# Performance work log

Hardware: AMD Instinct MI355X
Metric: run time of the kernel (lower is better)

## Reference

```python
import jax, jax.numpy as jnp
import numpy as np

N = 100000   # nodes
E = 400000   # edges
R = 237      # relations
D = 200      # feature dim (dims=[200,200,200])
B = 4096     # triple batch
L = 2        # num GAT layers
ALPHA = 0.01 # leaky-relu slope


def setup_inputs() -> dict:
    key = jax.random.key(0)
    ks = jax.random.split(key, 11)
    return dict(
        ent_embed=jax.random.normal(ks[0], (N, D), jnp.float32),
        rel_embed=jax.random.normal(ks[1], (R, D), jnp.float32),
        W_gat=jax.random.normal(ks[2], (L, D, D), jnp.float32) * 0.1,
        att_a=jax.random.normal(ks[3], (L, 2 * D), jnp.float32) * 0.1,
        W_hw=jax.random.normal(ks[4], (D, D), jnp.float32) * 0.1,
        b_hw=jax.random.normal(ks[5], (1, D), jnp.float32) * 0.1,
        edge_src=jax.random.randint(ks[6], (E,), 0, N),
        edge_dst=jax.random.randint(ks[7], (E,), 0, N),
        batch_h=jax.random.randint(ks[8], (B,), 0, N),
        batch_r=jax.random.randint(ks[9], (B,), 0, R),
        batch_t=jax.random.randint(ks[10], (B,), 0, N),
    )


def _gat_layer(x, W, a, src, dst):
    # x: [N,D], W: [D,D], a: [2D]
    Wh = x @ W                                  # [N,D]
    s_src = Wh @ a[:D]                          # [N] source score
    s_dst = Wh @ a[D:]                          # [N] dest score
    e = jax.nn.leaky_relu(s_src[src] + s_dst[dst], ALPHA)  # [E]
    # segment softmax over incoming edges of each destination node
    m = jax.ops.segment_max(e, dst, num_segments=N)
    m = jax.lax.stop_gradient(jnp.where(jnp.isfinite(m), m, 0.0))
    ex = jnp.exp(e - m[dst])
    denom = jax.ops.segment_sum(ex, dst, num_segments=N)
    att = ex / jnp.maximum(denom[dst], 1e-9)    # [E]
    out = jax.ops.segment_sum(att[:, None] * Wh[src], dst, num_segments=N)  # [N,D]
    return jax.nn.sigmoid(out)                  # act = torch.sigmoid, 1 head, concat=False


def reference(ent_embed, rel_embed, W_gat, att_a, W_hw, b_hw,
              edge_src, edge_dst, batch_h, batch_r, batch_t):
    x = ent_embed
    for i in range(L):
        gat_out = _gat_layer(x, W_gat[i], att_a[i], edge_src, edge_dst)
        # highway gate: sigma = sigmoid(x W + b); shared W,b across layers
        sigma = jax.nn.sigmoid(x @ W_hw + b_hw)
        x = sigma * gat_out + (1.0 - sigma) * x
    h = x[batch_h]
    r = rel_embed[batch_r]
    t = x[batch_t]
    return (h, r, t)
```

## Files before the change

kernel.cpp:

```cpp
#include <hip/hip_runtime.h>
#include <math.h>

#define NNODES 100000
#define NEDGES 400000
#define DIM    200
#define NB     4096
#define NL     2
#define ALPHA  0.01f
#define D4     (DIM/4)
#define NPAD   100096
#define KPAD   224
#define NKS    7
#define NCF    26
#define NBB    (2*NB)

typedef __attribute__((ext_vector_type(8))) short short8;
typedef __attribute__((ext_vector_type(4))) float f32x4;

__device__ __forceinline__ float sigm(float v) { return 1.0f / (1.0f + expf(-v)); }
__device__ __forceinline__ unsigned short f2bf(float f) {
    unsigned u = __float_as_uint(f);
    unsigned r = u + 0x7fff + ((u >> 16) & 1);
    return (unsigned short)(r >> 16);
}
__device__ __forceinline__ float bflo(unsigned u) { return __uint_as_float(u << 16); }
__device__ __forceinline__ float bfhi(unsigned u) { return __uint_as_float(u & 0xffff0000u); }

__global__ __launch_bounds__(256) void zero2_k(int* __restrict__ a, int* __restrict__ b)
{
    int i = blockIdx.x * 256 + threadIdx.x;
    if (i < NNODES) { a[i] = 0; b[i] = 0; }
}

__global__ __launch_bounds__(256) void convscore_k(const float* __restrict__ xin,
                                                   const float* __restrict__ wvl,
                                                   unsigned short* __restrict__ ap,
                                                   float* __restrict__ s_src,
                                                   float* __restrict__ s_dst)
{
    int gt = blockIdx.x * 256 + threadIdx.x;
    int row = gt >> 5, hl = gt & 31;
    if (row >= NPAD) return;

    float ps = 0.f, pd = 0.f;
    if (hl < 28) {
        uint4 o = make_uint4(0u, 0u, 0u, 0u);
        if (row < NNODES && hl < 25) {
            size_t base = (size_t)row * D4 + hl * 2;
            float4 x0 = ((const float4*)xin)[base];
            float4 x1 = ((const float4*)xin)[base + 1];
            o.x = (unsigned)f2bf(x0.x) | ((unsigned)f2bf(x0.y) << 16);
            o.y = (unsigned)f2bf(x0.z) | ((unsigned)f2bf(x0.w) << 16);
            o.z = (unsigned)f2bf(x1.x) | ((unsigned)f2bf(x1.y) << 16);
            o.w = (unsigned)f2bf(x1.z) | ((unsigned)f2bf(x1.w) << 16);
            float4 s0 = ((const float4*)wvl)[hl * 2];
            float4 s1 = ((const float4*)wvl)[hl * 2 + 1];
            float4 d0 = ((const float4*)(wvl + DIM))[hl * 2];
            float4 d1 = ((const float4*)(wvl + DIM))[hl * 2 + 1];
            ps = x0.x*s0.x + x0.y*s0.y + x0.z*s0.z + x0.w*s0.w
               + x1.x*s1.x + x1.y*s1.y + x1.z*s1.z + x1.w*s1.w;
            pd = x0.x*d0.x + x0.y*d0.y + x0.z*d0.z + x0.w*d0.w
               + x1.x*d1.x + x1.y*d1.y + x1.z*d1.z + x1.w*d1.w;
        }
        ((uint4*)ap)[(size_t)row * 28 + hl] = o;
    }
#pragma unroll
    for (int m = 16; m; m >>= 1) {
        ps += __shfl_xor(ps, m, 32);
        pd += __shfl_xor(pd, m, 32);
    }
    if (hl == 0 && row < NNODES) { s_src[row] = ps; s_dst[row] = pd; }
}

__global__ void wpack_k(const float* __restrict__ Wg, const float* __restrict__ Whw,
                        unsigned short* __restrict__ wp)
{
    int t = blockIdx.x * 256 + threadIdx.x;
    if (t >= NKS * NCF * 64) return;
    int l = t & 63, cf = (t >> 6) % NCF, ks = t / (NCF * 64);
    int col = (cf % 13) * 16 + (l & 15);
    const float* W = (cf < 13) ? Wg : Whw;
    unsigned rr[4];
#pragma unroll
    for (int j = 0; j < 4; ++j) {
        int ka = ks * 32 + (l >> 4) * 8 + 2 * j;
        float fa = (ka < DIM && col < DIM) ? W[ka * DIM + col] : 0.f;
        float fb = (ka + 1 < DIM && col < DIM) ? W[(ka + 1) * DIM + col] : 0.f;
        rr[j] = (unsigned)f2bf(fa) | ((unsigned)f2bf(fb) << 16);
    }
    ((uint4*)wp)[t] = make_uint4(rr[0], rr[1], rr[2], rr[3]);
}

__global__ void wvec_k(const float* __restrict__ Wg, const float* __restrict__ aa,
                       float* __restrict__ wv)
{
    int t = blockIdx.x * 256 + threadIdx.x;
    if (t >= NL * 2 * DIM) return;
    int l = t / (2 * DIM), sd = (t / DIM) % 2, k = t % DIM;
    const float* W = Wg + (size_t)l * DIM * DIM + (size_t)k * DIM;
    const float* av = aa + (size_t)l * 2 * DIM + sd * DIM;
    float s = 0.f;
    for (int c = 0; c < DIM; ++c) s = fmaf(W[c], av[c], s);
    wv[t] = s;
}

template<int CFBASE, int INDIRECT>
__global__ __launch_bounds__(448) void gemm_half_k(const unsigned short* __restrict__ Apack,
                                                   const unsigned short* __restrict__ Wpack,
                                                   const float* __restrict__ bhw,
                                                   unsigned short* __restrict__ outb,
                                                   const int* __restrict__ Lrow,
                                                   const int* __restrict__ nLp,
                                                   int nfix)
{
    int nrows = nLp ? *nLp : nfix;
    int rowbase = blockIdx.x * 32;
    if (rowbase >= nrows) return;

    int tid = threadIdx.x;
    int w = tid >> 6;
    int l = tid & 63;
    int cgrp = l >> 4, cidx = l & 15;
    int cf0 = CFBASE + 2 * w;
    int cf1 = CFBASE + 2 * w + 1;
    int cf1l = (cf1 < NCF) ? cf1 : (NCF - 1);

    const short8* Bp = (const short8*)Wpack + l;
    short8 b0[NKS], b1[NKS];
#pragma unroll
    for (int ks = 0; ks < NKS; ++ks) {
        b0[ks] = Bp[(ks * NCF + cf0) * 64];
        b1[ks] = Bp[(ks * NCF + cf1l) * 64];
    }

    int ar0 = rowbase + cidx, ar1 = rowbase + 16 + cidx;
    if (INDIRECT) {
        ar0 = Lrow[min(ar0, nrows - 1)];
        ar1 = Lrow[min(ar1, nrows - 1)];
    }
    const short8* Ap0 = (const short8*)(Apack + (size_t)ar0 * KPAD + cgrp * 8);
    const short8* Ap1 = (const short8*)(Apack + (size_t)ar1 * KPAD + cgrp * 8);

    f32x4 acc00 = (f32x4){0.f,0.f,0.f,0.f}, acc01 = acc00, acc10 = acc00, acc11 = acc00;

    short8 a0[2], a1[2];
    a0[0] = Ap0[0];
    a1[0] = Ap1[0];

#pragma unroll
    for (int ks = 0; ks < NKS; ++ks) {
        const int cur = ks & 1, nxt = cur ^ 1;
        if (ks + 1 < NKS) {
            a0[nxt] = Ap0[(ks + 1) * 4];
            a1[nxt] = Ap1[(ks + 1) * 4];
        }
        acc00 = __builtin_amdgcn_mfma_f32_16x16x32_bf16(a0[cur], b0[ks], acc00, 0, 0, 0);
        acc01 = __builtin_amdgcn_mfma_f32_16x16x32_bf16(a0[cur], b1[ks], acc01, 0, 0, 0);
        acc10 = __builtin_amdgcn_mfma_f32_16x16x32_bf16(a1[cur], b0[ks], acc10, 0, 0, 0);
        acc11 = __builtin_amdgcn_mfma_f32_16x16x32_bf16(a1[cur], b1[ks], acc11, 0, 0, 0);
    }

#pragma unroll
    for (int cc = 0; cc < 2; ++cc) {
        int cf = cc ? cf1 : cf0;
        if (cf >= CFBASE + 13) continue;
        int col = (cf - CFBASE) * 16 + cidx;
        if (col >= DIM) continue;
        f32x4 ar_0 = cc ? acc01 : acc00;
        f32x4 ar_1 = cc ? acc11 : acc10;
        if (CFBASE == 0) {
#pragma unroll
            for (int r = 0; r < 4; ++r) {
                int row = rowbase + cgrp * 4 + r;
                if (row < nrows) outb[(size_t)row * DIM + col] = f2bf(ar_0[r]);
                row += 16;
                if (row < nrows) outb[(size_t)row * DIM + col] = f2bf(ar_1[r]);
            }
        } else {
            float bb2 = bhw[col];
#pragma unroll
            for (int r = 0; r < 4; ++r) {
                int row = rowbase + cgrp * 4 + r;
                if (row < nrows) outb[(size_t)row * DIM + col] = f2bf(sigm(ar_0[r] + bb2));
                row += 16;
                if (row < nrows) outb[(size_t)row * DIM + col] = f2bf(sigm(ar_1[r] + bb2));
            }
        }
    }
}

__global__ void hist_k(const int* __restrict__ dst, int* __restrict__ deg)
{
    int e = blockIdx.x * blockDim.x + threadIdx.x;
    if (e < NEDGES) atomicAdd(&deg[dst[e]], 1);
}

__global__ void scan1_k(const int* __restrict__ deg, int* __restrict__ rs,
                        int* __restrict__ bsum)
{
    __shared__ int tmp[256];
    int tid = threadIdx.x;
    int i = blockIdx.x * 256 + tid;
    int v = (i < NNODES) ? deg[i] : 0;
    tmp[tid] = v; __syncthreads();
#pragma unroll
    for (int off = 1; off < 256; off <<= 1) {
        int t = (tid >= off) ? tmp[tid - off] : 0;
        __syncthreads();
        tmp[tid] += t;
        __syncthreads();
    }
    if (i < NNODES) rs[i] = tmp[tid] - v;
    if (tid == 255) bsum[blockIdx.x] = tmp[255];
}

__global__ void scan2_k(int* __restrict__ bsum, int nb)
{
    __shared__ int tmp[512];
    int tid = threadIdx.x;
    int v = (tid < nb) ? bsum[tid] : 0;
    tmp[tid] = v; __syncthreads();
#pragma unroll
    for (int off = 1; off < 512; off <<= 1) {
        int t = (tid >= off) ? tmp[tid - off] : 0;
        __syncthreads();
        tmp[tid] += t;
        __syncthreads();
    }
    if (tid < nb) bsum[tid] = tmp[tid] - v;
}

__global__ void scan3_k(int* __restrict__ rs, const int* __restrict__ bsum,
                        int* __restrict__ cursor)
{
    int i = blockIdx.x * 256 + threadIdx.x;
    if (i < NNODES) {
        int v = rs[i] + bsum[blockIdx.x];
        rs[i] = v;
        cursor[i] = v;
    }
    if (i == 0) rs[NNODES] = NEDGES;
}

__global__ void scatter_k(const int* __restrict__ src, const int* __restrict__ dst,
                          int* __restrict__ cursor, int* __restrict__ csr_src)
{
    int e = blockIdx.x * blockDim.x + threadIdx.x;
    if (e >= NEDGES) return;
    int d = dst[e];
    int p = atomicAdd(&cursor[d], 1);
    csr_src[p] = src[e];
}

__global__ void mark_k(const int* __restrict__ bh, const int* __restrict__ bt,
                       const int* __restrict__ rs, const int* __restrict__ csr_src,
                       int* __restrict__ mask)
{
    int e = blockIdx.x * 256 + threadIdx.x;
    if (e >= NBB) return;
    int node = (e < NB) ? bh[e] : bt[e - NB];
    mask[node] = 1;
    int b = rs[node], en = rs[node + 1];
    for (int j = b; j < en; ++j) mask[csr_src[j]] = 1;
}

__global__ void listfill_k(const int* __restrict__ posl, const int* __restrict__ bsum2,
                           const int* __restrict__ mask, int* __restrict__ Lrow,
                           int* __restrict__ inv, int* __restrict__ nLp)
{
    int i = blockIdx.x * 256 + threadIdx.x;
    if (i >= NNODES) return;
    int pos = posl[i] + bsum2[blockIdx.x];
    if (mask[i]) { Lrow[pos] = i; inv[i] = pos; }
    if (i == NNODES - 1) *nLp = pos + mask[i];
}

__global__ __launch_bounds__(256) void agg3c_k(const int* __restrict__ csr_src,
                                               const int* __restrict__ rs,
                                               const float* __restrict__ s_src,
                                               const float* __restrict__ s_dst,
                                               const unsigned short* __restrict__ whb,
                                               const unsigned short* __restrict__ sgc,
                                               unsigned short* __restrict__ apack,
                                               const int* __restrict__ Lrow,
                                               const int* __restrict__ nLp,
                                               const float* __restrict__ wvn,
                                               float* __restrict__ o_ssrc,
                                               float* __restrict__ o_sdst)
{
    int gt = blockIdx.x * 256 + threadIdx.x;
    int lidx = gt >> 5;
    int hl = gt & 31;
    if (lidx >= *nLp) return;
    int node = Lrow[lidx];

    int beg = rs[node], end = rs[node + 1];
    float sd = s_dst[node];

    float m = -3.4e38f;
    for (int j = beg + hl; j < end; j += 32) {
        float v = s_src[csr_src[j]] + sd;
        v = v > 0.f ? v : ALPHA * v;
        m = fmaxf(m, v);
    }
#pragma unroll
    for (int s = 16; s; s >>= 1) m = fmaxf(m, __shfl_xor(m, s, 32));
    float sum = 0.f;
    for (int j = beg + hl; j < end; j += 32) {
        float v = s_src[csr_src[j]] + sd;
        v = v > 0.f ? v : ALPHA * v;
        sum += expf(v - m);
    }
#pragma unroll
    for (int s = 16; s; s >>= 1) sum += __shfl_xor(sum, s, 32);
    float inv_ = 1.f / fmaxf(sum, 1e-9f);

    float ps = 0.f, pd = 0.f;
    if (hl < 25) {
        float av[8] = {0.f, 0.f, 0.f, 0.f, 0.f, 0.f, 0.f, 0.f};
        int j = beg;
        for (; j + 1 < end; j += 2) {
            int n0 = csr_src[j], n1 = csr_src[j + 1];
            float v0 = s_src[n0] + sd, v1 = s_src[n1] + sd;
            v0 = v0 > 0.f ? v0 : ALPHA * v0;
            v1 = v1 > 0.f ? v1 : ALPHA * v1;
            float c0 = expf(v0 - m) * inv_, c1 = expf(v1 - m) * inv_;
            uint4 w0 = ((const uint4*)whb)[(size_t)n0 * 25 + hl];
            uint4 w1 = ((const uint4*)whb)[(size_t)n1 * 25 + hl];
            av[0] = fmaf(c0, bflo(w0.x), av[0]); av[0] = fmaf(c1, bflo(w1.x), av[0]);
            av[1] = fmaf(c0, bfhi(w0.x), av[1]); av[1] = fmaf(c1, bfhi(w1.x), av[1]);
            av[2] = fmaf(c0, bflo(w0.y), av[2]); av[2] = fmaf(c1, bflo(w1.y), av[2]);
            av[3] = fmaf(c0, bfhi(w0.y), av[3]); av[3] = fmaf(c1, bfhi(w1.y), av[3]);
            av[4] = fmaf(c0, bflo(w0.z), av[4]); av[4] = fmaf(c1, bflo(w1.z), av[4]);
            av[5] = fmaf(c0, bfhi(w0.z), av[5]); av[5] = fmaf(c1, bfhi(w1.z), av[5]);
            av[6] = fmaf(c0, bflo(w0.w), av[6]); av[6] = fmaf(c1, bflo(w1.w), av[6]);
            av[7] = fmaf(c0, bfhi(w0.w), av[7]); av[7] = fmaf(c1, bfhi(w1.w), av[7]);
        }
        if (j < end) {
            int n0 = csr_src[j];
            float v0 = s_src[n0] + sd;
            v0 = v0 > 0.f ? v0 : ALPHA * v0;
            float c0 = expf(v0 - m) * inv_;
            uint4 w0 = ((const uint4*)whb)[(size_t)n0 * 25 + hl];
            av[0] = fmaf(c0, bflo(w0.x), av[0]);
            av[1] = fmaf(c0, bfhi(w0.x), av[1]);
            av[2] = fmaf(c0, bflo(w0.y), av[2]);
            av[3] = fmaf(c0, bfhi(w0.y), av[3]);
            av[4] = fmaf(c0, bflo(w0.z), av[4]);
            av[5] = fmaf(c0, bfhi(w0.z), av[5]);
            av[6] = fmaf(c0, bflo(w0.w), av[6]);
            av[7] = fmaf(c0, bfhi(w0.w), av[7]);
        }

        uint4 sv = ((const uint4*)sgc)[(size_t)lidx * 25 + hl];
        uint4 xv = ((const uint4*)apack)[(size_t)node * 28 + hl];
        float4 o0, o1;
        float s0;
        s0 = bflo(sv.x); o0.x = s0 * sigm(av[0]) + (1.f - s0) * bflo(xv.x);
        s0 = bfhi(sv.x); o0.y = s0 * sigm(av[1]) + (1.f - s0) * bfhi(xv.x);
        s0 = bflo(sv.y); o0.z = s0 * sigm(av[2]) + (1.f - s0) * bflo(xv.y);
        s0 = bfhi(sv.y); o0.w = s0 * sigm(av[3]) + (1.f - s0) * bfhi(xv.y);
        s0 = bflo(sv.z); o1.x = s0 * sigm(av[4]) + (1.f - s0) * bflo(xv.z);
        s0 = bfhi(sv.z); o1.y = s0 * sigm(av[5]) + (1.f - s0) * bfhi(xv.z);
        s0 = bflo(sv.w); o1.z = s0 * sigm(av[6]) + (1.f - s0) * bflo(xv.w);
        s0 = bfhi(sv.w); o1.w = s0 * sigm(av[7]) + (1.f - s0) * bfhi(xv.w);

        unsigned r0 = (unsigned)f2bf(o0.x) | ((unsigned)f2bf(o0.y) << 16);
        unsigned r1 = (unsigned)f2bf(o0.z) | ((unsigned)f2bf(o0.w) << 16);
        unsigned r2 = (unsigned)f2bf(o1.x) | ((unsigned)f2bf(o1.y) << 16);
        unsigned r3 = (unsigned)f2bf(o1.z) | ((unsigned)f2bf(o1.w) << 16);
        ((uint4*)apack)[(size_t)node * 28 + hl] = make_uint4(r0, r1, r2, r3);

        float4 ws0 = ((const float4*)wvn)[hl * 2];
        float4 ws1 = ((const float4*)wvn)[hl * 2 + 1];
        float4 wd0 = ((const float4*)(wvn + DIM))[hl * 2];
        float4 wd1 = ((const float4*)(wvn + DIM))[hl * 2 + 1];
        ps = o0.x*ws0.x + o0.y*ws0.y + o0.z*ws0.z + o0.w*ws0.w
           + o1.x*ws1.x + o1.y*ws1.y + o1.z*ws1.z + o1.w*ws1.w;
        pd = o0.x*wd0.x + o0.y*wd0.y + o0.z*wd0.z + o0.w*wd0.w
           + o1.x*wd1.x + o1.y*wd1.y + o1.z*wd1.z + o1.w*wd1.w;
    }
#pragma unroll
    for (int s = 16; s; s >>= 1) {
        ps += __shfl_xor(ps, s, 32);
        pd += __shfl_xor(pd, s, 32);
    }
    if (hl == 0) { o_ssrc[node] = ps; o_sdst[node] = pd; }
}

__global__ void gatherx_k(const unsigned short* __restrict__ apack,
                          const int* __restrict__ bh, const int* __restrict__ bt,
                          unsigned short* __restrict__ bx)
{
    int i = blockIdx.x * 256 + threadIdx.x;
    if (i >= NBB * 28) return;
    int e = i / 28, q = i - e * 28;
    int node = (e < NB) ? bh[e] : bt[e - NB];
    ((uint4*)bx)[i] = ((const uint4*)apack)[(size_t)node * 28 + q];
}

__global__ void relcopy_k(const float* __restrict__ rel, const int* __restrict__ br,
                          float* __restrict__ out)
{
    int i = blockIdx.x * 256 + threadIdx.x;
    if (i >= NB * D4) return;
    int row = i / D4, c = i - row * D4;
    ((float4*)out)[(size_t)(NB + row) * D4 + c] = ((const float4*)rel)[(size_t)br[row] * D4 + c];
}

__global__ __launch_bounds__(256) void agg4_k(const int* __restrict__ csr_src,
                                              const int* __restrict__ rs,
                                              const float* __restrict__ s_src,
                                              const float* __restrict__ s_dst,
                                              const unsigned short* __restrict__ whc,
                                              const int* __restrict__ inv,
                                              const unsigned short* __restrict__ sgbatch,
                                              const unsigned short* __restrict__ bxpack,
                                              const int* __restrict__ bh,
                                              const int* __restrict__ bt,
                                              float* __restrict__ out)
{
    int gt = blockIdx.x * 256 + threadIdx.x;
    int e = gt >> 5;
    int hl = gt & 31;
    if (e >= NBB) return;
    int node = (e < NB) ? bh[e] : bt[e - NB];
    int orow = (e < NB) ? e : (2 * NB + (e - NB));

    int beg = rs[node], end = rs[node + 1];
    float sd = s_dst[node];

    float m = -3.4e38f;
    for (int j = beg + hl; j < end; j += 32) {
        float v = s_src[csr_src[j]] + sd;
        v = v > 0.f ? v : ALPHA * v;
        m = fmaxf(m, v);
    }
#pragma unroll
    for (int s = 16; s; s >>= 1) m = fmaxf(m, __shfl_xor(m, s, 32));
    float sum = 0.f;
    for (int j = beg + hl; j < end; j += 32) {
        float v = s_src[csr_src[j]] + sd;
        v = v > 0.f ? v : ALPHA * v;
        sum += expf(v - m);
    }
#pragma unroll
    for (int s = 16; s; s >>= 1) sum += __shfl_xor(sum, s, 32);
    float inv_ = 1.f / fmaxf(sum, 1e-9f);

    if (hl < 25) {
        float av[8] = {0.f, 0.f, 0.f, 0.f, 0.f, 0.f, 0.f, 0.f};
        int j = beg;
        for (; j + 1 < end; j += 2) {
            int n0 = csr_src[j], n1 = csr_src[j + 1];
            float v0 = s_src[n0] + sd, v1 = s_src[n1] + sd;
            v0 = v0 > 0.f ? v0 : ALPHA * v0;
            v1 = v1 > 0.f ? v1 : ALPHA * v1;
            float c0 = expf(v0 - m) * inv_, c1 = expf(v1 - m) * inv_;
            uint4 w0 = ((const uint4*)whc)[(size_t)inv[n0] * 25 + hl];
            uint4 w1 = ((const uint4*)whc)[(size_t)inv[n1] * 25 + hl];
            av[0] = fmaf(c0, bflo(w0.x), av[0]); av[0] = fmaf(c1, bflo(w1.x), av[0]);
            av[1] = fmaf(c0, bfhi(w0.x), av[1]); av[1] = fmaf(c1, bfhi(w1.x), av[1]);
            av[2] = fmaf(c0, bflo(w0.y), av[2]); av[2] = fmaf(c1, bflo(w1.y), av[2]);
            av[3] = fmaf(c0, bfhi(w0.y), av[3]); av[3] = fmaf(c1, bfhi(w1.y), av[3]);
            av[4] = fmaf(c0, bflo(w0.z), av[4]); av[4] = fmaf(c1, bflo(w1.z), av[4]);
            av[5] = fmaf(c0, bfhi(w0.z), av[5]); av[5] = fmaf(c1, bfhi(w1.z), av[5]);
            av[6] = fmaf(c0, bflo(w0.w), av[6]); av[6] = fmaf(c1, bflo(w1.w), av[6]);
            av[7] = fmaf(c0, bfhi(w0.w), av[7]); av[7] = fmaf(c1, bfhi(w1.w), av[7]);
        }
        if (j < end) {
            int n0 = csr_src[j];
            float v0 = s_src[n0] + sd;
            v0 = v0 > 0.f ? v0 : ALPHA * v0;
            float c0 = expf(v0 - m) * inv_;
            uint4 w0 = ((const uint4*)whc)[(size_t)inv[n0] * 25 + hl];
            av[0] = fmaf(c0, bflo(w0.x), av[0]);
            av[1] = fmaf(c0, bfhi(w0.x), av[1]);
            av[2] = fmaf(c0, bflo(w0.y), av[2]);
            av[3] = fmaf(c0, bfhi(w0.y), av[3]);
            av[4] = fmaf(c0, bflo(w0.z), av[4]);
            av[5] = fmaf(c0, bfhi(w0.z), av[5]);
            av[6] = fmaf(c0, bflo(w0.w), av[6]);
            av[7] = fmaf(c0, bfhi(w0.w), av[7]);
        }

        uint4 sv = ((const uint4*)sgbatch)[(size_t)e * 25 + hl];
        uint4 xv = ((const uint4*)bxpack)[(size_t)e * 28 + hl];
        float4 o0, o1;
        float s0;
        s0 = bflo(sv.x); o0.x = s0 * sigm(av[0]) + (1.f - s0) * bflo(xv.x);
        s0 = bfhi(sv.x); o0.y = s0 * sigm(av[1]) + (1.f - s0) * bfhi(xv.x);
        s0 = bflo(sv.y); o0.z = s0 * sigm(av[2]) + (1.f - s0) * bflo(xv.y);
        s0 = bfhi(sv.y); o0.w = s0 * sigm(av[3]) + (1.f - s0) * bfhi(xv.y);
        s0 = bflo(sv.z); o1.x = s0 * sigm(av[4]) + (1.f - s0) * bflo(xv.z);
        s0 = bfhi(sv.z); o1.y = s0 * sigm(av[5]) + (1.f - s0) * bfhi(xv.z);
        s0 = bflo(sv.w); o1.z = s0 * sigm(av[6]) + (1.f - s0) * bflo(xv.w);
        s0 = bfhi(sv.w); o1.w = s0 * sigm(av[7]) + (1.f - s0) * bfhi(xv.w);

        size_t base = (size_t)orow * D4 + hl * 2;
        ((float4*)out)[base]     = o0;
        ((float4*)out)[base + 1] = o1;
    }
}

extern "C" void kernel_launch(void* const* d_in, const int* in_sizes, int n_in,
                              void* d_out, int out_size, void* d_ws, size_t ws_size,
                              hipStream_t stream)
{
    const float* ent = (const float*)d_in[0];
    const float* rel = (const float*)d_in[1];
    const float* Wg  = (const float*)d_in[2];
    const float* aa  = (const float*)d_in[3];
    const float* Whw = (const float*)d_in[4];
    const float* bhw = (const float*)d_in[5];
    const int* esrc  = (const int*)d_in[6];
    const int* edst  = (const int*)d_in[7];
    const int* bh    = (const int*)d_in[8];
    const int* br    = (const int*)d_in[9];
    const int* bt    = (const int*)d_in[10];
    float* out = (float*)d_out;

    char* p = (char*)d_ws;
    auto carve = [&](size_t bytes) { char* r = p; p += (bytes + 63) & ~(size_t)63; return r; };
    unsigned short* whb     = (unsigned short*)carve((size_t)NNODES * DIM * 2);
    unsigned short* whc     = (unsigned short*)carve((size_t)NNODES * DIM * 2);
    unsigned short* sgc     = (unsigned short*)carve((size_t)NNODES * DIM * 2);
    unsigned short* apack   = (unsigned short*)carve((size_t)NPAD * KPAD * 2);
    unsigned short* bxpack  = (unsigned short*)carve((size_t)NBB * KPAD * 2);
    unsigned short* sgbatch = (unsigned short*)carve((size_t)NBB * DIM * 2);
    unsigned short* wp0     = (unsigned short*)carve((size_t)NKS * NCF * 64 * 16);
    unsigned short* wp1     = (unsigned short*)carve((size_t)NKS * NCF * 64 * 16);
    float* wv    = (float*)carve(NL * 2 * DIM * 4);
    float* ss0   = (float*)carve(NNODES * 4);
    float* sd0   = (float*)carve(NNODES * 4);
    float* ss1   = (float*)carve(NNODES * 4);
    float* sd1   = (float*)carve(NNODES * 4);
    int* deg     = (int*)carve(NNODES * 4);
    int* rs      = (int*)carve((NNODES + 1) * 4);
    int* cursor  = (int*)carve(NNODES * 4);
    int* bsum    = (int*)carve(512 * 4);
    int* csr_src = (int*)carve(NEDGES * 4);
    int* mask    = (int*)carve(NNODES * 4);
    int* posl    = (int*)carve(NNODES * 4);
    int* Lrow    = (int*)carve(NNODES * 4);
    int* inv     = (int*)carve(NNODES * 4);
    int* bsum2   = (int*)carve(512 * 4);
    int* nLp     = (int*)carve(64);

    const int NBLK = (NNODES + 255) / 256;

    zero2_k<<<NBLK, 256, 0, stream>>>(deg, mask);

    hist_k<<<(NEDGES + 255) / 256, 256, 0, stream>>>(edst, deg);
    scan1_k<<<NBLK, 256, 0, stream>>>(deg, rs, bsum);
    scan2_k<<<1, 512, 0, stream>>>(bsum, NBLK);
    scan3_k<<<NBLK, 256, 0, stream>>>(rs, bsum, cursor);
    scatter_k<<<(NEDGES + 255) / 256, 256, 0, stream>>>(esrc, edst, cursor, csr_src);

    mark_k<<<(NBB + 255) / 256, 256, 0, stream>>>(bh, bt, rs, csr_src, mask);
    scan1_k<<<NBLK, 256, 0, stream>>>(mask, posl, bsum2);
    scan2_k<<<1, 512, 0, stream>>>(bsum2, NBLK);
    listfill_k<<<NBLK, 256, 0, stream>>>(posl, bsum2, mask, Lrow, inv, nLp);

    wpack_k<<<(NKS * NCF * 64 + 255) / 256, 256, 0, stream>>>(Wg, Whw, wp0);
    wpack_k<<<(NKS * NCF * 64 + 255) / 256, 256, 0, stream>>>(Wg + (size_t)DIM * DIM, Whw, wp1);
    wvec_k<<<(NL * 2 * DIM + 255) / 256, 256, 0, stream>>>(Wg, aa, wv);

    convscore_k<<<(NPAD * 32) / 256, 256, 0, stream>>>(ent, wv, apack, ss0, sd0);

    const int GFULL = NPAD / 32;

    gemm_half_k<0, 0><<<GFULL, 448, 0, stream>>>(apack, wp0, bhw, whb, nullptr, nullptr, NNODES);
    gemm_half_k<13, 1><<<GFULL, 448, 0, stream>>>(apack, wp0, bhw, sgc, Lrow, nLp, 0);
    agg3c_k<<<(NNODES * 32) / 256, 256, 0, stream>>>(csr_src, rs, ss0, sd0, whb, sgc,
                                                     apack, Lrow, nLp, wv + 2 * DIM, ss1, sd1);

    gemm_half_k<0, 1><<<GFULL, 448, 0, stream>>>(apack, wp1, bhw, whc, Lrow, nLp, 0);
    gatherx_k<<<(NBB * 28 + 255) / 256, 256, 0, stream>>>(apack, bh, bt, bxpack);
    gemm_half_k<13, 0><<<NBB / 32, 448, 0, stream>>>(bxpack, wp1, bhw, sgbatch, nullptr, nullptr, NBB);
    relcopy_k<<<(NB * D4 + 255) / 256, 256, 0, stream>>>(rel, br, out);
    agg4_k<<<(NBB * 32) / 256, 256, 0, stream>>>(csr_src, rs, ss1, sd1, whc, inv,
                                                 sgbatch, bxpack, bh, bt, out);
}
```

Measured before the change: 229.4 us.

## Fuse CSR graph build into one cooperative kernel and merge small prep kernels

```diff
diff --git a/kernel.cpp b/kernel.cpp
--- a/kernel.cpp
+++ b/kernel.cpp
@@ -1,5 +1,8 @@
 #include <hip/hip_runtime.h>
+#include <hip/hip_cooperative_groups.h>
 #include <math.h>
+
+namespace cg = cooperative_groups;
 
 #define NNODES 100000
 #define NEDGES 400000
@@ -13,6 +16,7 @@
 #define NKS    7
 #define NCF    26
 #define NBB    (2*NB)
+#define NBLK   ((NNODES + 255) / 256)
 
 typedef __attribute__((ext_vector_type(8))) short short8;
 typedef __attribute__((ext_vector_type(4))) float f32x4;
@@ -26,10 +30,100 @@
 __device__ __forceinline__ float bflo(unsigned u) { return __uint_as_float(u << 16); }
 __device__ __forceinline__ float bfhi(unsigned u) { return __uint_as_float(u & 0xffff0000u); }
 
-__global__ __launch_bounds__(256) void zero2_k(int* __restrict__ a, int* __restrict__ b)
-{
-    int i = blockIdx.x * 256 + threadIdx.x;
-    if (i < NNODES) { a[i] = 0; b[i] = 0; }
+__global__ __launch_bounds__(256) void graph_k(
+    const int* __restrict__ esrc, const int* __restrict__ edst,
+    const int* __restrict__ bh, const int* __restrict__ bt,
+    int* __restrict__ deg, int* __restrict__ rs, int* __restrict__ cursor,
+    int* __restrict__ bsum, int* __restrict__ csr_src,
+    int* __restrict__ mask, int* __restrict__ bsum2,
+    int* __restrict__ Lrow, int* __restrict__ inv, int* __restrict__ nLp)
+{
+    cg::grid_group grid = cg::this_grid();
+    const int tid = threadIdx.x;
+    const int gid = blockIdx.x * 256 + tid;
+    const int nthr = gridDim.x * 256;
+    __shared__ int tmp[256];
+
+    if (gid < NNODES) { deg[gid] = 0; mask[gid] = 0; }
+    grid.sync();
+
+    for (int e = gid; e < NEDGES; e += nthr) atomicAdd(&deg[edst[e]], 1);
+    grid.sync();
+
+    {
+        int v = (gid < NNODES) ? deg[gid] : 0;
+        tmp[tid] = v; __syncthreads();
+#pragma unroll
+        for (int off = 1; off < 256; off <<= 1) {
+            int t = (tid >= off) ? tmp[tid - off] : 0;
+            __syncthreads();
+            tmp[tid] += t;
+            __syncthreads();
+        }
+        int le = tmp[tid] - v;
+        if (tid == 255) bsum[blockIdx.x] = tmp[255];
+        grid.sync();
+        int acc = 0;
+        for (int j = tid; j < (int)blockIdx.x; j += 256) acc += bsum[j];
+        __syncthreads();
+        tmp[tid] = acc; __syncthreads();
+#pragma unroll
+        for (int off = 128; off; off >>= 1) {
+            if (tid < off) tmp[tid] += tmp[tid + off];
+            __syncthreads();
+        }
+        int off0 = tmp[0];
+        __syncthreads();
+        if (gid < NNODES) { int r = le + off0; rs[gid] = r; cursor[gid] = r; }
+        if (gid == 0) rs[NNODES] = NEDGES;
+    }
+    grid.sync();
+
+    for (int e = gid; e < NEDGES; e += nthr) {
+        int d = edst[e];
+        int p = atomicAdd(&cursor[d], 1);
+        csr_src[p] = esrc[e];
+    }
+    grid.sync();
+
+    for (int e = gid; e < NBB; e += nthr) {
+        int node = (e < NB) ? bh[e] : bt[e - NB];
+        mask[node] = 1;
+        int b = rs[node], en = rs[node + 1];
+        for (int j = b; j < en; ++j) mask[csr_src[j]] = 1;
+    }
+    grid.sync();
+
+    {
+        int v = (gid < NNODES) ? mask[gid] : 0;
+        tmp[tid] = v; __syncthreads();
+#pragma unroll
+        for (int off = 1; off < 256; off <<= 1) {
+            int t = (tid >= off) ? tmp[tid - off] : 0;
+            __syncthreads();
+            tmp[tid] += t;
+            __syncthreads();
+        }
+        int le = tmp[tid] - v;
+        if (tid == 255) bsum2[blockIdx.x] = tmp[255];
+        grid.sync();
+        int acc = 0;
+        for (int j = tid; j < (int)blockIdx.x; j += 256) acc += bsum2[j];
+        __syncthreads();
+        tmp[tid] = acc; __syncthreads();
+#pragma unroll
+        for (int off = 128; off; off >>= 1) {
+            if (tid < off) tmp[tid] += tmp[tid + off];
+            __syncthreads();
+        }
+        int off0 = tmp[0];
+        __syncthreads();
+        if (gid < NNODES) {
+            int pos = le + off0;
+            if (v) { Lrow[pos] = gid; inv[gid] = pos; }
+            if (gid == NNODES - 1) *nLp = pos + v;
+        }
+    }
 }
 
 __global__ __launch_bounds__(256) void convscore_k(const float* __restrict__ xin,
@@ -72,36 +166,42 @@
     if (hl == 0 && row < NNODES) { s_src[row] = ps; s_dst[row] = pd; }
 }
 
-__global__ void wpack_k(const float* __restrict__ Wg, const float* __restrict__ Whw,
-                        unsigned short* __restrict__ wp)
-{
-    int t = blockIdx.x * 256 + threadIdx.x;
-    if (t >= NKS * NCF * 64) return;
-    int l = t & 63, cf = (t >> 6) % NCF, ks = t / (NCF * 64);
-    int col = (cf % 13) * 16 + (l & 15);
-    const float* W = (cf < 13) ? Wg : Whw;
-    unsigned rr[4];
-#pragma unroll
-    for (int j = 0; j < 4; ++j) {
-        int ka = ks * 32 + (l >> 4) * 8 + 2 * j;
-        float fa = (ka < DIM && col < DIM) ? W[ka * DIM + col] : 0.f;
-        float fb = (ka + 1 < DIM && col < DIM) ? W[(ka + 1) * DIM + col] : 0.f;
-        rr[j] = (unsigned)f2bf(fa) | ((unsigned)f2bf(fb) << 16);
-    }
-    ((uint4*)wp)[t] = make_uint4(rr[0], rr[1], rr[2], rr[3]);
-}
-
-__global__ void wvec_k(const float* __restrict__ Wg, const float* __restrict__ aa,
-                       float* __restrict__ wv)
-{
-    int t = blockIdx.x * 256 + threadIdx.x;
-    if (t >= NL * 2 * DIM) return;
-    int l = t / (2 * DIM), sd = (t / DIM) % 2, k = t % DIM;
-    const float* W = Wg + (size_t)l * DIM * DIM + (size_t)k * DIM;
-    const float* av = aa + (size_t)l * 2 * DIM + sd * DIM;
-    float s = 0.f;
-    for (int c = 0; c < DIM; ++c) s = fmaf(W[c], av[c], s);
-    wv[t] = s;
+__global__ __launch_bounds__(256) void prep_k(const float* __restrict__ Wg,
+                                              const float* __restrict__ Whw,
+                                              const float* __restrict__ aa,
+                                              unsigned short* __restrict__ wp0,
+                                              unsigned short* __restrict__ wp1,
+                                              float* __restrict__ wv)
+{
+    int t0 = blockIdx.x * 256 + threadIdx.x;
+    const int WP = NKS * NCF * 64;
+    if (t0 < 2 * WP) {
+        int pk = (t0 >= WP) ? 1 : 0;
+        int t = t0 - pk * WP;
+        const float* Wgl = Wg + (size_t)pk * DIM * DIM;
+        unsigned short* wp = pk ? wp1 : wp0;
+        int l = t & 63, cf = (t >> 6) % NCF, ks = t / (NCF * 64);
+        int col = (cf % 13) * 16 + (l & 15);
+        const float* W = (cf < 13) ? Wgl : Whw;
+        unsigned rr[4];
+#pragma unroll
+        for (int j = 0; j < 4; ++j) {
+            int ka = ks * 32 + (l >> 4) * 8 + 2 * j;
+            float fa = (ka < DIM && col < DIM) ? W[ka * DIM + col] : 0.f;
+            float fb = (ka + 1 < DIM && col < DIM) ? W[(ka + 1) * DIM + col] : 0.f;
+            rr[j] = (unsigned)f2bf(fa) | ((unsigned)f2bf(fb) << 16);
+        }
+        ((uint4*)wp)[t] = make_uint4(rr[0], rr[1], rr[2], rr[3]);
+    } else {
+        int u = t0 - 2 * WP;
+        if (u >= NL * 2 * DIM) return;
+        int l = u / (2 * DIM), sd = (u / DIM) % 2, k = u % DIM;
+        const float* W = Wg + (size_t)l * DIM * DIM + (size_t)k * DIM;
+        const float* av = aa + (size_t)l * 2 * DIM + sd * DIM;
+        float s = 0.f;
+        for (int c = 0; c < DIM; ++c) s = fmaf(W[c], av[c], s);
+        wv[u] = s;
+    }
 }
 
 template<int CFBASE, int INDIRECT>
@@ -187,92 +287,6 @@
             }
         }
     }
-}
-
-__global__ void hist_k(const int* __restrict__ dst, int* __restrict__ deg)
-{
-    int e = blockIdx.x * blockDim.x + threadIdx.x;
-    if (e < NEDGES) atomicAdd(&deg[dst[e]], 1);
-}
-
-__global__ void scan1_k(const int* __restrict__ deg, int* __restrict__ rs,
-                        int* __restrict__ bsum)
-{
-    __shared__ int tmp[256];
-    int tid = threadIdx.x;
-    int i = blockIdx.x * 256 + tid;
-    int v = (i < NNODES) ? deg[i] : 0;
-    tmp[tid] = v; __syncthreads();
-#pragma unroll
-    for (int off = 1; off < 256; off <<= 1) {
-        int t = (tid >= off) ? tmp[tid - off] : 0;
-        __syncthreads();
-        tmp[tid] += t;
-        __syncthreads();
-    }
-    if (i < NNODES) rs[i] = tmp[tid] - v;
-    if (tid == 255) bsum[blockIdx.x] = tmp[255];
-}
-
-__global__ void scan2_k(int* __restrict__ bsum, int nb)
-{
-    __shared__ int tmp[512];
-    int tid = threadIdx.x;
-    int v = (tid < nb) ? bsum[tid] : 0;
-    tmp[tid] = v; __syncthreads();
-#pragma unroll
-    for (int off = 1; off < 512; off <<= 1) {
-        int t = (tid >= off) ? tmp[tid - off] : 0;
-        __syncthreads();
-        tmp[tid] += t;
-        __syncthreads();
-    }
-    if (tid < nb) bsum[tid] = tmp[tid] - v;
-}
-
-__global__ void scan3_k(int* __restrict__ rs, const int* __restrict__ bsum,
-                        int* __restrict__ cursor)
-{
-    int i = blockIdx.x * 256 + threadIdx.x;
-    if (i < NNODES) {
-        int v = rs[i] + bsum[blockIdx.x];
-        rs[i] = v;
-        cursor[i] = v;
-    }
-    if (i == 0) rs[NNODES] = NEDGES;
-}
-
-__global__ void scatter_k(const int* __restrict__ src, const int* __restrict__ dst,
-                          int* __restrict__ cursor, int* __restrict__ csr_src)
-{
-    int e = blockIdx.x * blockDim.x + threadIdx.x;
-    if (e >= NEDGES) return;
-    int d = dst[e];
-    int p = atomicAdd(&cursor[d], 1);
-    csr_src[p] = src[e];
-}
-
-__global__ void mark_k(const int* __restrict__ bh, const int* __restrict__ bt,
-                       const int* __restrict__ rs, const int* __restrict__ csr_src,
-                       int* __restrict__ mask)
-{
-    int e = blockIdx.x * 256 + threadIdx.x;
-    if (e >= NBB) return;
-    int node = (e < NB) ? bh[e] : bt[e - NB];
-    mask[node] = 1;
-    int b = rs[node], en = rs[node + 1];
-    for (int j = b; j < en; ++j) mask[csr_src[j]] = 1;
-}
-
-__global__ void listfill_k(const int* __restrict__ posl, const int* __restrict__ bsum2,
-                           const int* __restrict__ mask, int* __restrict__ Lrow,
-                           int* __restrict__ inv, int* __restrict__ nLp)
-{
-    int i = blockIdx.x * 256 + threadIdx.x;
-    if (i >= NNODES) return;
-    int pos = posl[i] + bsum2[blockIdx.x];
-    if (mask[i]) { Lrow[pos] = i; inv[i] = pos; }
-    if (i == NNODES - 1) *nLp = pos + mask[i];
 }
 
 __global__ __launch_bounds__(256) void agg3c_k(const int* __restrict__ csr_src,
@@ -388,24 +402,27 @@
     if (hl == 0) { o_ssrc[node] = ps; o_sdst[node] = pd; }
 }
 
-__global__ void gatherx_k(const unsigned short* __restrict__ apack,
-                          const int* __restrict__ bh, const int* __restrict__ bt,
-                          unsigned short* __restrict__ bx)
+__global__ __launch_bounds__(256) void gatherrel_k(const unsigned short* __restrict__ apack,
+                                                   const int* __restrict__ bh,
+                                                   const int* __restrict__ bt,
+                                                   unsigned short* __restrict__ bx,
+                                                   const float* __restrict__ rel,
+                                                   const int* __restrict__ br,
+                                                   float* __restrict__ out)
 {
     int i = blockIdx.x * 256 + threadIdx.x;
-    if (i >= NBB * 28) return;
-    int e = i / 28, q = i - e * 28;
-    int node = (e < NB) ? bh[e] : bt[e - NB];
-    ((uint4*)bx)[i] = ((const uint4*)apack)[(size_t)node * 28 + q];
-}
-
-__global__ void relcopy_k(const float* __restrict__ rel, const int* __restrict__ br,
-                          float* __restrict__ out)
-{
-    int i = blockIdx.x * 256 + threadIdx.x;
-    if (i >= NB * D4) return;
-    int row = i / D4, c = i - row * D4;
-    ((float4*)out)[(size_t)(NB + row) * D4 + c] = ((const float4*)rel)[(size_t)br[row] * D4 + c];
+    const int GX = NBB * 28;
+    if (i < GX) {
+        int e = i / 28, q = i - e * 28;
+        int node = (e < NB) ? bh[e] : bt[e - NB];
+        ((uint4*)bx)[i] = ((const uint4*)apack)[(size_t)node * 28 + q];
+    } else {
+        int u = i - GX;
+        if (u >= NB * D4) return;
+        int row = u / D4, c = u - row * D4;
+        ((float4*)out)[(size_t)(NB + row) * D4 + c] =
+            ((const float4*)rel)[(size_t)br[row] * D4 + c];
+    }
 }
 
 __global__ __launch_bounds__(256) void agg4_k(const int* __restrict__ csr_src,
@@ -541,30 +558,19 @@
     int* bsum    = (int*)carve(512 * 4);
     int* csr_src = (int*)carve(NEDGES * 4);
     int* mask    = (int*)carve(NNODES * 4);
-    int* posl    = (int*)carve(NNODES * 4);
     int* Lrow    = (int*)carve(NNODES * 4);
     int* inv     = (int*)carve(NNODES * 4);
     int* bsum2   = (int*)carve(512 * 4);
     int* nLp     = (int*)carve(64);
 
-    const int NBLK = (NNODES + 255) / 256;
-
-    zero2_k<<<NBLK, 256, 0, stream>>>(deg, mask);
-
-    hist_k<<<(NEDGES + 255) / 256, 256, 0, stream>>>(edst, deg);
-    scan1_k<<<NBLK, 256, 0, stream>>>(deg, rs, bsum);
-    scan2_k<<<1, 512, 0, stream>>>(bsum, NBLK);
-    scan3_k<<<NBLK, 256, 0, stream>>>(rs, bsum, cursor);
-    scatter_k<<<(NEDGES + 255) / 256, 256, 0, stream>>>(esrc, edst, cursor, csr_src);
-
-    mark_k<<<(NBB + 255) / 256, 256, 0, stream>>>(bh, bt, rs, csr_src, mask);
-    scan1_k<<<NBLK, 256, 0, stream>>>(mask, posl, bsum2);
-    scan2_k<<<1, 512, 0, stream>>>(bsum2, NBLK);
-    listfill_k<<<NBLK, 256, 0, stream>>>(posl, bsum2, mask, Lrow, inv, nLp);
-
-    wpack_k<<<(NKS * NCF * 64 + 255) / 256, 256, 0, stream>>>(Wg, Whw, wp0);
-    wpack_k<<<(NKS * NCF * 64 + 255) / 256, 256, 0, stream>>>(Wg + (size_t)DIM * DIM, Whw, wp1);
-    wvec_k<<<(NL * 2 * DIM + 255) / 256, 256, 0, stream>>>(Wg, aa, wv);
+    void* gargs[] = { (void*)&esrc, (void*)&edst, (void*)&bh, (void*)&bt,
+                      (void*)&deg, (void*)&rs, (void*)&cursor, (void*)&bsum,
+                      (void*)&csr_src, (void*)&mask, (void*)&bsum2,
+                      (void*)&Lrow, (void*)&inv, (void*)&nLp };
+    hipLaunchCooperativeKernel((void*)graph_k, dim3(NBLK), dim3(256), gargs, 0, stream);
+
+    prep_k<<<(2 * NKS * NCF * 64 + NL * 2 * DIM + 255) / 256, 256, 0, stream>>>(
+        Wg, Whw, aa, wp0, wp1, wv);
 
     convscore_k<<<(NPAD * 32) / 256, 256, 0, stream>>>(ent, wv, apack, ss0, sd0);
 
@@ -576,9 +582,9 @@
                                                      apack, Lrow, nLp, wv + 2 * DIM, ss1, sd1);
 
     gemm_half_k<0, 1><<<GFULL, 448, 0, stream>>>(apack, wp1, bhw, whc, Lrow, nLp, 0);
-    gatherx_k<<<(NBB * 28 + 255) / 256, 256, 0, stream>>>(apack, bh, bt, bxpack);
+    gatherrel_k<<<(NBB * 28 + NB * D4 + 255) / 256, 256, 0, stream>>>(
+        apack, bh, bt, bxpack, rel, br, out);
     gemm_half_k<13, 0><<<NBB / 32, 448, 0, stream>>>(bxpack, wp1, bhw, sgbatch, nullptr, nullptr, NBB);
-    relcopy_k<<<(NB * D4 + 255) / 256, 256, 0, stream>>>(rel, br, out);
     agg4_k<<<(NBB * 32) / 256, 256, 0, stream>>>(csr_src, rs, ss1, sd1, whc, inv,
                                                  sgbatch, bxpack, bh, bt, out);
 }
```

Result: slower. 525.5 us (+129.1%).
